# Optimization experiments

Measured on AMD Instinct MI355X. Metric: run time of the kernel, lower is better.

## Reference

```python
import jax, jax.numpy as jnp
import numpy as np

N_EMBD = 64
N_HEAD = 8
HEAD_SIZE = N_EMBD // N_HEAD  # 8
BLOCK_SIZE = 64
B = 4096
SCALE = N_EMBD ** (-0.5)  # NOTE: source scales by C**-0.5 with C=n_embd, not head_size
EPS = 1e-5


def setup_inputs() -> dict:
    key = jax.random.key(0)
    ks = jax.random.split(key, 12)
    s = 0.02
    return {
        "x": jax.random.normal(ks[0], (B, BLOCK_SIZE, N_EMBD), jnp.float32),
        # per-head q/k/v projections packed as [C, H, hs] (no bias in source)
        "Wq": jax.random.normal(ks[1], (N_EMBD, N_HEAD, HEAD_SIZE), jnp.float32) * s,
        "Wk": jax.random.normal(ks[2], (N_EMBD, N_HEAD, HEAD_SIZE), jnp.float32) * s,
        "Wv": jax.random.normal(ks[3], (N_EMBD, N_HEAD, HEAD_SIZE), jnp.float32) * s,
        "Wo": jax.random.normal(ks[4], (N_EMBD, N_EMBD), jnp.float32) * s,
        "bo": jnp.zeros((N_EMBD,), jnp.float32),
        "W1": jax.random.normal(ks[5], (N_EMBD, 4 * N_EMBD), jnp.float32) * s,
        "b1": jnp.zeros((4 * N_EMBD,), jnp.float32),
        "W2": jax.random.normal(ks[6], (4 * N_EMBD, N_EMBD), jnp.float32) * s,
        "b2": jnp.zeros((N_EMBD,), jnp.float32),
        "g1": jnp.ones((N_EMBD,), jnp.float32),
        "be1": jnp.zeros((N_EMBD,), jnp.float32),
        "g2": jnp.ones((N_EMBD,), jnp.float32),
        "be2": jnp.zeros((N_EMBD,), jnp.float32),
    }


def _layernorm(x, g, b):
    mu = jnp.mean(x, axis=-1, keepdims=True)
    var = jnp.mean(jnp.square(x - mu), axis=-1, keepdims=True)
    return (x - mu) * jax.lax.rsqrt(var + EPS) * g + b


def reference(x, Wq, Wk, Wv, Wo, bo, W1, b1, W2, b2, g1, be1, g2, be2):
    Bb, T, C = x.shape
    # --- multi-head causal self-attention (dropout = identity in eval) ---
    h = _layernorm(x, g1, be1)
    q = jnp.einsum('btc,chd->bhtd', h, Wq)
    k = jnp.einsum('btc,chd->bhtd', h, Wk)
    v = jnp.einsum('btc,chd->bhtd', h, Wv)
    wei = jnp.einsum('bhtd,bhsd->bhts', q, k) * SCALE
    mask = jnp.tril(jnp.ones((T, T), dtype=bool))
    wei = jnp.where(mask, wei, -jnp.inf)
    wei = jax.nn.softmax(wei, axis=-1)
    attn = jnp.einsum('bhts,bhsd->bhtd', wei, v)
    attn = attn.transpose(0, 2, 1, 3).reshape(Bb, T, C)  # concat heads
    x = x + attn @ Wo + bo
    # --- feed-forward ---
    h2 = _layernorm(x, g2, be2)
    ff = jax.nn.relu(h2 @ W1 + b1) @ W2 + b2
    return x + ff
```

## Files before the change

kernel.cpp:

```cpp
#include <hip/hip_runtime.h>
#include <hip/hip_bf16.h>


typedef __attribute__((ext_vector_type(8))) short short8;
typedef __attribute__((ext_vector_type(4))) float f32x4;

#if __has_builtin(__builtin_amdgcn_exp2f)
#define EXP2F(x) __builtin_amdgcn_exp2f(x)
#else
#define EXP2F(x) __expf((x) * 0.69314718056f)
#endif
#if __has_builtin(__builtin_amdgcn_rcpf)
#define RCPF(x) __builtin_amdgcn_rcpf(x)
#else
#define RCPF(x) (1.0f / (x))
#endif

#define ST  72
#define STU 264
#define OH  0
#define OQ  4608
#define OKK 9216
#define OV  13824
#define OP  18576
#define OU  9216
#define NSH 26112

__device__ __forceinline__ short f2bf(float f) {
    unsigned int u = __float_as_uint(f);
    u += 0x7fffu + ((u >> 16) & 1u);
    return (short)(u >> 16);
}
__device__ __forceinline__ unsigned pk2(float a, float b) {
    float2 t; t.x = a; t.y = b;
    __hip_bfloat162 h = __float22bfloat162_rn(t);
    unsigned u; __builtin_memcpy(&u, &h, 4); return u;
}
__device__ __forceinline__ f32x4 mfma16(short8 a, short8 b, f32x4 c) {
    return __builtin_amdgcn_mfma_f32_16x16x32_bf16(a, b, c, 0, 0, 0);
}

__global__ __launch_bounds__(256) void prepack_kernel(
    const float* __restrict__ Wq, const float* __restrict__ Wk,
    const float* __restrict__ Wv, const float* __restrict__ Wo,
    const float* __restrict__ W1, const float* __restrict__ W2,
    short* __restrict__ ws)
{
    int gid = blockIdx.x * 256 + threadIdx.x;
    int lane = gid & 63;
    int fid  = gid >> 6;
    int quad = lane >> 4, nn = lane & 15;
    short8 o;
    if (fid < 24) {
        int tile = fid >> 1, ks = fid & 1;
        const float* Ws = (tile < 4) ? Wq : ((tile < 8) ? Wk : Wv);
        float scale = (tile < 4) ? 0.18033688011f : 1.0f;
        int col = (tile & 3) * 16 + nn;
#pragma unroll
        for (int j = 0; j < 8; ++j)
            o[j] = f2bf(Ws[(ks * 32 + quad * 8 + j) * 64 + col] * scale);
    } else if (fid < 32) {
        int idx = fid - 24, nt = idx >> 1, ks = idx & 1;
#pragma unroll
        for (int j = 0; j < 8; ++j)
            o[j] = f2bf(Wo[(ks * 32 + quad * 8 + j) * 64 + nt * 16 + nn]);
    } else if (fid < 64) {
        int idx = fid - 32, c = idx >> 3, tile = (idx >> 1) & 3, ks = idx & 1;
#pragma unroll
        for (int j = 0; j < 8; ++j)
            o[j] = f2bf(W1[(ks * 32 + quad * 8 + j) * 256 + c * 64 + tile * 16 + nn]);
    } else {
        int idx = fid - 64, c = idx >> 3, nt = (idx >> 1) & 3, ks = idx & 1;
#pragma unroll
        for (int j = 0; j < 8; ++j)
            o[j] = f2bf(W2[(c * 64 + ks * 32 + quad * 8 + j) * 64 + nt * 16 + nn]);
    }
    *(short8*)(ws + (size_t)gid * 8) = o;
}

__global__ __launch_bounds__(256, 3) void block_kernel(
    const float* __restrict__ x,
    const float* __restrict__ bo,
    const float* __restrict__ b1,
    const float* __restrict__ b2,
    const float* __restrict__ g1, const float* __restrict__ be1,
    const float* __restrict__ g2, const float* __restrict__ be2,
    const short8* __restrict__ WB,
    float* __restrict__ out)
{
    __shared__ short sm[NSH];
    const int tid  = threadIdx.x;
    const int wv   = tid >> 6;
    const int lane = tid & 63;
    const int quad = lane >> 4;
    const int nn   = lane & 15;
    const int t_my = wv * 16 + nn;
    const int b    = blockIdx.x;
    const float* xb = x + (size_t)b * 4096;
    const f32x4 zf = {0.f, 0.f, 0.f, 0.f};
    const short8 z8 = {0, 0, 0, 0, 0, 0, 0, 0};

    if (tid < 144) sm[OV + 64 * ST + tid] = (tid < ST) ? (short)0x3F80 : (short)0;
    float xr[16];
    float gv[4], bv[4];
#pragma unroll
    for (int nt = 0; nt < 4; ++nt) { gv[nt] = g1[nt * 16 + nn]; bv[nt] = be1[nt * 16 + nn]; }
#pragma unroll
    for (int nt = 0; nt < 4; ++nt)
#pragma unroll
        for (int r = 0; r < 4; ++r)
            xr[nt * 4 + r] = xb[(wv * 16 + quad * 4 + r) * 64 + nt * 16 + nn];
#pragma unroll
    for (int r = 0; r < 4; ++r) {
        float s1 = 0.f, s2 = 0.f;
#pragma unroll
        for (int nt = 0; nt < 4; ++nt) { float v = xr[nt * 4 + r]; s1 += v; s2 += v * v; }
        s1 += __shfl_xor(s1, 1); s1 += __shfl_xor(s1, 2); s1 += __shfl_xor(s1, 4); s1 += __shfl_xor(s1, 8);
        s2 += __shfl_xor(s2, 1); s2 += __shfl_xor(s2, 2); s2 += __shfl_xor(s2, 4); s2 += __shfl_xor(s2, 8);
        float mu = s1 * 0.015625f;
        float rstd = rsqrtf(s2 * 0.015625f - mu * mu + 1e-5f);
        int base = OH + (wv * 16 + quad * 4 + r) * ST + nn;
        float v0 = (xr[0 * 4 + r] - mu) * rstd * gv[0] + bv[0];
        float v1 = (xr[1 * 4 + r] - mu) * rstd * gv[1] + bv[1];
        float v2 = (xr[2 * 4 + r] - mu) * rstd * gv[2] + bv[2];
        float v3 = (xr[3 * 4 + r] - mu) * rstd * gv[3] + bv[3];
        unsigned p01 = pk2(v0, v1), p23 = pk2(v2, v3);
        sm[base]      = (short)(p01 & 0xffff);
        sm[base + 16] = (short)(p01 >> 16);
        sm[base + 32] = (short)(p23 & 0xffff);
        sm[base + 48] = (short)(p23 >> 16);
    }

    {
        short8 hf0 = *(const short8*)&sm[OH + t_my * ST + quad * 8];
        short8 hf1 = *(const short8*)&sm[OH + t_my * ST + 32 + quad * 8];
#pragma unroll
        for (int jt = 0; jt < 4; ++jt) {
            f32x4 a = mfma16(WB[(size_t)(jt * 2 + 0) * 64 + lane], hf0, zf);
            a = mfma16(WB[(size_t)(jt * 2 + 1) * 64 + lane], hf1, a);
            uint2 w; w.x = pk2(a[0], a[1]); w.y = pk2(a[2], a[3]);
            *(uint2*)&sm[OQ + t_my * ST + jt * 16 + quad * 4] = w;
        }
#pragma unroll
        for (int jt = 0; jt < 4; ++jt) {
            f32x4 a = mfma16(WB[(size_t)((4 + jt) * 2 + 0) * 64 + lane], hf0, zf);
            a = mfma16(WB[(size_t)((4 + jt) * 2 + 1) * 64 + lane], hf1, a);
            uint2 w; w.x = pk2(a[0], a[1]); w.y = pk2(a[2], a[3]);
            *(uint2*)&sm[OKK + t_my * ST + jt * 16 + quad * 4] = w;
        }
#pragma unroll
        for (int dt = 0; dt < 4; ++dt) {
            f32x4 a = mfma16(hf0, WB[(size_t)((8 + dt) * 2 + 0) * 64 + lane], zf);
            a = mfma16(hf1, WB[(size_t)((8 + dt) * 2 + 1) * 64 + lane], a);
            uint2 w; w.x = pk2(a[0], a[1]); w.y = pk2(a[2], a[3]);
            *(uint2*)&sm[OV + (dt * 16 + nn) * ST + wv * 16 + quad * 4] = w;
        }
    }
    __syncthreads();

    const bool keep0 = (quad * 4 + 0) <= nn, keep1 = (quad * 4 + 1) <= nn;
    const bool keep2 = (quad * 4 + 2) <= nn, keep3 = (quad * 4 + 3) <= nn;
    const int arow_base = (nn < 8) ? nn : ((nn == 8) ? 64 : 65);
    const int arow_step = (nn < 8) ? 8 : 0;
    const int nks = (wv < 2) ? 1 : 2;
    const int zhi = nks * 2;
#pragma unroll 1
    for (int h = 0; h < 8; ++h) {
        short8 bq = z8;
        if (quad == 0) bq = *(const short8*)&sm[OQ + t_my * ST + h * 8];
        for (int mt = 0; mt <= wv; ++mt) {
            short8 ak = z8;
            if (quad == 0) ak = *(const short8*)&sm[OKK + (mt * 16 + nn) * ST + h * 8];
            f32x4 s = mfma16(ak, bq, zf);
            float e0 = EXP2F(s[0]), e1 = EXP2F(s[1]), e2 = EXP2F(s[2]), e3 = EXP2F(s[3]);
            if (mt == wv) {
                e0 = keep0 ? e0 : 0.f; e1 = keep1 ? e1 : 0.f;
                e2 = keep2 ? e2 : 0.f; e3 = keep3 ? e3 : 0.f;
            }
            uint2 w; w.x = pk2(e0, e1); w.y = pk2(e2, e3);
            *(uint2*)&sm[OP + t_my * ST + mt * 16 + quad * 4] = w;
        }
        for (int mt = wv + 1; mt < zhi; ++mt) {
            uint2 w; w.x = 0u; w.y = 0u;
            *(uint2*)&sm[OP + t_my * ST + mt * 16 + quad * 4] = w;
        }
        const int arow = arow_base + h * arow_step;
        f32x4 pv = zf;
        for (int ks = 0; ks < nks; ++ks) {
            short8 av = *(const short8*)&sm[OV + arow * ST + ks * 32 + quad * 8];
            short8 bp = *(const short8*)&sm[OP + t_my * ST + ks * 32 + quad * 8];
            pv = mfma16(av, bp, pv);
        }
        float denom = __shfl(pv[0], 32 + nn);
        float rd = RCPF(denom);
        if (quad < 2) {
            uint2 w; w.x = pk2(pv[0] * rd, pv[1] * rd); w.y = pk2(pv[2] * rd, pv[3] * rd);
            *(uint2*)&sm[OH + t_my * ST + h * 8 + quad * 4] = w;
        }
    }

    {
        short8 aa0 = *(const short8*)&sm[OH + t_my * ST + quad * 8];
        short8 aa1 = *(const short8*)&sm[OH + t_my * ST + 32 + quad * 8];
#pragma unroll
        for (int nt = 0; nt < 4; ++nt) {
            f32x4 oa = mfma16(aa0, WB[(size_t)(24 + nt * 2 + 0) * 64 + lane], zf);
            oa = mfma16(aa1, WB[(size_t)(24 + nt * 2 + 1) * 64 + lane], oa);
            float bov = bo[nt * 16 + nn];
#pragma unroll
            for (int r = 0; r < 4; ++r) xr[nt * 4 + r] += oa[r] + bov;
        }
    }
#pragma unroll
    for (int nt = 0; nt < 4; ++nt) { gv[nt] = g2[nt * 16 + nn]; bv[nt] = be2[nt * 16 + nn]; }
#pragma unroll
    for (int r = 0; r < 4; ++r) {
        float s1 = 0.f, s2 = 0.f;
#pragma unroll
        for (int nt = 0; nt < 4; ++nt) { float v = xr[nt * 4 + r]; s1 += v; s2 += v * v; }
        s1 += __shfl_xor(s1, 1); s1 += __shfl_xor(s1, 2); s1 += __shfl_xor(s1, 4); s1 += __shfl_xor(s1, 8);
        s2 += __shfl_xor(s2, 1); s2 += __shfl_xor(s2, 2); s2 += __shfl_xor(s2, 4); s2 += __shfl_xor(s2, 8);
        float mu = s1 * 0.015625f;
        float rstd = rsqrtf(s2 * 0.015625f - mu * mu + 1e-5f);
        int base = OQ + (wv * 16 + quad * 4 + r) * ST + nn;
        float v0 = (xr[0 * 4 + r] - mu) * rstd * gv[0] + bv[0];
        float v1 = (xr[1 * 4 + r] - mu) * rstd * gv[1] + bv[1];
        float v2 = (xr[2 * 4 + r] - mu) * rstd * gv[2] + bv[2];
        float v3 = (xr[3 * 4 + r] - mu) * rstd * gv[3] + bv[3];
        unsigned p01 = pk2(v0, v1), p23 = pk2(v2, v3);
        sm[base]      = (short)(p01 & 0xffff);
        sm[base + 16] = (short)(p01 >> 16);
        sm[base + 32] = (short)(p23 & 0xffff);
        sm[base + 48] = (short)(p23 >> 16);
    }

    short8 h2f0 = *(const short8*)&sm[OQ + t_my * ST + quad * 8];
    short8 h2f1 = *(const short8*)&sm[OQ + t_my * ST + 32 + quad * 8];
    __syncthreads();
#pragma unroll
    for (int c = 0; c < 4; ++c)
#pragma unroll
        for (int tile = 0; tile < 4; ++tile) {
            int fid = 32 + c * 8 + tile * 2;
            f32x4 u = mfma16(WB[(size_t)fid * 64 + lane], h2f0, zf);
            u = mfma16(WB[(size_t)(fid + 1) * 64 + lane], h2f1, u);
            const float4 bb = *(const float4*)&b1[c * 64 + tile * 16 + quad * 4];
            float u0 = fmaxf(u[0] + bb.x, 0.f), u1 = fmaxf(u[1] + bb.y, 0.f);
            float u2 = fmaxf(u[2] + bb.z, 0.f), u3 = fmaxf(u[3] + bb.w, 0.f);
            uint2 w; w.x = pk2(u0, u1); w.y = pk2(u2, u3);
            *(uint2*)&sm[OU + t_my * STU + c * 64 + tile * 16 + quad * 4] = w;
        }
    short8 uf[8];
#pragma unroll
    for (int ks = 0; ks < 8; ++ks)
        uf[ks] = *(const short8*)&sm[OU + t_my * STU + ks * 32 + quad * 8];
    f32x4 fa[4];
#pragma unroll
    for (int nt = 0; nt < 4; ++nt) fa[nt] = zf;
#pragma unroll
    for (int nt = 0; nt < 4; ++nt)
#pragma unroll
        for (int ks = 0; ks < 8; ++ks)
            fa[nt] = mfma16(uf[ks], WB[(size_t)(64 + (ks >> 1) * 8 + nt * 2 + (ks & 1)) * 64 + lane], fa[nt]);

    float* ob = out + (size_t)b * 4096;
#pragma unroll
    for (int nt = 0; nt < 4; ++nt) {
        float b2v = b2[nt * 16 + nn];
#pragma unroll
        for (int r = 0; r < 4; ++r)
            ob[(wv * 16 + quad * 4 + r) * 64 + nt * 16 + nn] = xr[nt * 4 + r] + fa[nt][r] + b2v;
    }
}

extern "C" void kernel_launch(void* const* d_in, const int* in_sizes, int n_in,
                              void* d_out, int out_size, void* d_ws, size_t ws_size,
                              hipStream_t stream) {
    const float* x   = (const float*)d_in[0];
    const float* Wq  = (const float*)d_in[1];
    const float* Wk  = (const float*)d_in[2];
    const float* Wv  = (const float*)d_in[3];
    const float* Wo  = (const float*)d_in[4];
    const float* bo  = (const float*)d_in[5];
    const float* W1  = (const float*)d_in[6];
    const float* b1  = (const float*)d_in[7];
    const float* W2  = (const float*)d_in[8];
    const float* b2  = (const float*)d_in[9];
    const float* g1  = (const float*)d_in[10];
    const float* be1 = (const float*)d_in[11];
    const float* g2  = (const float*)d_in[12];
    const float* be2 = (const float*)d_in[13];
    short* ws = (short*)d_ws;
    prepack_kernel<<<dim3(24), dim3(256), 0, stream>>>(Wq, Wk, Wv, Wo, W1, W2, ws);
    const int nb = in_sizes[0] / 4096;
    block_kernel<<<dim3(nb), dim3(256), 0, stream>>>(
        x, bo, b1, b2, g1, be1, g2, be2, (const short8*)ws, (float*)d_out);
}
```

Baseline: 206.4 us.

## Shrink shared memory footprint to raise occupancy to four blocks per CU

Q is kept in registers and broadcast through lane shuffles instead of being staged in shared memory. The FFN hidden activations are processed in two halves of 128 columns, so the U buffer shrinks and the second matmul is interleaved with the first. Shared memory drops from about 52KB to about 37KB, and launch bounds are raised to four blocks per CU to hide latency. The trade-offs are extra shuffles per head and tighter register pressure, and the weight prepack is relaunched with 64-thread blocks.

```diff
diff --git a/kernel.cpp b/kernel.cpp
--- a/kernel.cpp
+++ b/kernel.cpp
@@ -17,14 +17,13 @@
 #endif
 
 #define ST  72
-#define STU 264
+#define STU 136
 #define OH  0
-#define OQ  4608
-#define OKK 9216
-#define OV  13824
-#define OP  18576
-#define OU  9216
-#define NSH 26112
+#define OKK 4608
+#define OV  9216
+#define OP  13896
+#define OU  4608
+#define NSH 18504
 
 __device__ __forceinline__ short f2bf(float f) {
     unsigned int u = __float_as_uint(f);
@@ -40,13 +39,13 @@
     return __builtin_amdgcn_mfma_f32_16x16x32_bf16(a, b, c, 0, 0, 0);
 }
 
-__global__ __launch_bounds__(256) void prepack_kernel(
+__global__ __launch_bounds__(64) void prepack_kernel(
     const float* __restrict__ Wq, const float* __restrict__ Wk,
     const float* __restrict__ Wv, const float* __restrict__ Wo,
     const float* __restrict__ W1, const float* __restrict__ W2,
     short* __restrict__ ws)
 {
-    int gid = blockIdx.x * 256 + threadIdx.x;
+    int gid = blockIdx.x * 64 + threadIdx.x;
     int lane = gid & 63;
     int fid  = gid >> 6;
     int quad = lane >> 4, nn = lane & 15;
@@ -78,7 +77,7 @@
     *(short8*)(ws + (size_t)gid * 8) = o;
 }
 
-__global__ __launch_bounds__(256, 3) void block_kernel(
+__global__ __launch_bounds__(256, 4) void block_kernel(
     const float* __restrict__ x,
     const float* __restrict__ bo,
     const float* __restrict__ b1,
@@ -100,7 +99,7 @@
     const f32x4 zf = {0.f, 0.f, 0.f, 0.f};
     const short8 z8 = {0, 0, 0, 0, 0, 0, 0, 0};
 
-    if (tid < 144) sm[OV + 64 * ST + tid] = (tid < ST) ? (short)0x3F80 : (short)0;
+    if (tid < ST) sm[OV + 64 * ST + tid] = (short)0x3F80;
     float xr[16];
     float gv[4], bv[4];
 #pragma unroll
@@ -120,17 +119,12 @@
         float mu = s1 * 0.015625f;
         float rstd = rsqrtf(s2 * 0.015625f - mu * mu + 1e-5f);
         int base = OH + (wv * 16 + quad * 4 + r) * ST + nn;
-        float v0 = (xr[0 * 4 + r] - mu) * rstd * gv[0] + bv[0];
-        float v1 = (xr[1 * 4 + r] - mu) * rstd * gv[1] + bv[1];
-        float v2 = (xr[2 * 4 + r] - mu) * rstd * gv[2] + bv[2];
-        float v3 = (xr[3 * 4 + r] - mu) * rstd * gv[3] + bv[3];
-        unsigned p01 = pk2(v0, v1), p23 = pk2(v2, v3);
-        sm[base]      = (short)(p01 & 0xffff);
-        sm[base + 16] = (short)(p01 >> 16);
-        sm[base + 32] = (short)(p23 & 0xffff);
-        sm[base + 48] = (short)(p23 >> 16);
-    }
-
+#pragma unroll
+        for (int nt = 0; nt < 4; ++nt)
+            sm[base + nt * 16] = f2bf((xr[nt * 4 + r] - mu) * rstd * gv[nt] + bv[nt]);
+    }
+
+    unsigned qp[8];
     {
         short8 hf0 = *(const short8*)&sm[OH + t_my * ST + quad * 8];
         short8 hf1 = *(const short8*)&sm[OH + t_my * ST + 32 + quad * 8];
@@ -138,8 +132,8 @@
         for (int jt = 0; jt < 4; ++jt) {
             f32x4 a = mfma16(WB[(size_t)(jt * 2 + 0) * 64 + lane], hf0, zf);
             a = mfma16(WB[(size_t)(jt * 2 + 1) * 64 + lane], hf1, a);
-            uint2 w; w.x = pk2(a[0], a[1]); w.y = pk2(a[2], a[3]);
-            *(uint2*)&sm[OQ + t_my * ST + jt * 16 + quad * 4] = w;
+            qp[jt * 2 + 0] = pk2(a[0], a[1]);
+            qp[jt * 2 + 1] = pk2(a[2], a[3]);
         }
 #pragma unroll
         for (int jt = 0; jt < 4; ++jt) {
@@ -160,14 +154,23 @@
 
     const bool keep0 = (quad * 4 + 0) <= nn, keep1 = (quad * 4 + 1) <= nn;
     const bool keep2 = (quad * 4 + 2) <= nn, keep3 = (quad * 4 + 3) <= nn;
-    const int arow_base = (nn < 8) ? nn : ((nn == 8) ? 64 : 65);
+    const int arow_base = (nn < 8) ? nn : 64;
     const int arow_step = (nn < 8) ? 8 : 0;
     const int nks = (wv < 2) ? 1 : 2;
     const int zhi = nks * 2;
 #pragma unroll 1
     for (int h = 0; h < 8; ++h) {
-        short8 bq = z8;
-        if (quad == 0) bq = *(const short8*)&sm[OQ + t_my * ST + h * 8];
+        short8 bq;
+        {
+            int qsA = ((h & 1) * 2) * 16 + nn, qsB = qsA + 16;
+            int qi = (h >> 1) * 2;
+            union { unsigned u[4]; short8 s; } bb;
+            bb.u[0] = __shfl(qp[qi + 0], qsA);
+            bb.u[1] = __shfl(qp[qi + 1], qsA);
+            bb.u[2] = __shfl(qp[qi + 0], qsB);
+            bb.u[3] = __shfl(qp[qi + 1], qsB);
+            bq = bb.s;
+        }
         for (int mt = 0; mt <= wv; ++mt) {
             short8 ak = z8;
             if (quad == 0) ak = *(const short8*)&sm[OKK + (mt * 16 + nn) * ST + h * 8];
@@ -222,46 +225,42 @@
         s2 += __shfl_xor(s2, 1); s2 += __shfl_xor(s2, 2); s2 += __shfl_xor(s2, 4); s2 += __shfl_xor(s2, 8);
         float mu = s1 * 0.015625f;
         float rstd = rsqrtf(s2 * 0.015625f - mu * mu + 1e-5f);
-        int base = OQ + (wv * 16 + quad * 4 + r) * ST + nn;
-        float v0 = (xr[0 * 4 + r] - mu) * rstd * gv[0] + bv[0];
-        float v1 = (xr[1 * 4 + r] - mu) * rstd * gv[1] + bv[1];
-        float v2 = (xr[2 * 4 + r] - mu) * rstd * gv[2] + bv[2];
-        float v3 = (xr[3 * 4 + r] - mu) * rstd * gv[3] + bv[3];
-        unsigned p01 = pk2(v0, v1), p23 = pk2(v2, v3);
-        sm[base]      = (short)(p01 & 0xffff);
-        sm[base + 16] = (short)(p01 >> 16);
-        sm[base + 32] = (short)(p23 & 0xffff);
-        sm[base + 48] = (short)(p23 >> 16);
-    }
-
-    short8 h2f0 = *(const short8*)&sm[OQ + t_my * ST + quad * 8];
-    short8 h2f1 = *(const short8*)&sm[OQ + t_my * ST + 32 + quad * 8];
+        int base = OP + (wv * 16 + quad * 4 + r) * ST + nn;
+#pragma unroll
+        for (int nt = 0; nt < 4; ++nt)
+            sm[base + nt * 16] = f2bf((xr[nt * 4 + r] - mu) * rstd * gv[nt] + bv[nt]);
+    }
+    short8 h2f0 = *(const short8*)&sm[OP + t_my * ST + quad * 8];
+    short8 h2f1 = *(const short8*)&sm[OP + t_my * ST + 32 + quad * 8];
     __syncthreads();
-#pragma unroll
-    for (int c = 0; c < 4; ++c)
-#pragma unroll
-        for (int tile = 0; tile < 4; ++tile) {
-            int fid = 32 + c * 8 + tile * 2;
+
+    f32x4 fa[4];
+#pragma unroll
+    for (int nt = 0; nt < 4; ++nt) fa[nt] = zf;
+#pragma unroll
+    for (int c = 0; c < 2; ++c) {
+#pragma unroll
+        for (int tile = 0; tile < 8; ++tile) {
+            int gc = c * 8 + tile;
+            int fid = 32 + (gc >> 2) * 8 + (gc & 3) * 2;
             f32x4 u = mfma16(WB[(size_t)fid * 64 + lane], h2f0, zf);
             u = mfma16(WB[(size_t)(fid + 1) * 64 + lane], h2f1, u);
-            const float4 bb = *(const float4*)&b1[c * 64 + tile * 16 + quad * 4];
+            const float4 bb = *(const float4*)&b1[gc * 16 + quad * 4];
             float u0 = fmaxf(u[0] + bb.x, 0.f), u1 = fmaxf(u[1] + bb.y, 0.f);
             float u2 = fmaxf(u[2] + bb.z, 0.f), u3 = fmaxf(u[3] + bb.w, 0.f);
             uint2 w; w.x = pk2(u0, u1); w.y = pk2(u2, u3);
-            *(uint2*)&sm[OU + t_my * STU + c * 64 + tile * 16 + quad * 4] = w;
-        }
-    short8 uf[8];
-#pragma unroll
-    for (int ks = 0; ks < 8; ++ks)
-        uf[ks] = *(const short8*)&sm[OU + t_my * STU + ks * 32 + quad * 8];
-    f32x4 fa[4];
-#pragma unroll
-    for (int nt = 0; nt < 4; ++nt) fa[nt] = zf;
-#pragma unroll
-    for (int nt = 0; nt < 4; ++nt)
-#pragma unroll
-        for (int ks = 0; ks < 8; ++ks)
-            fa[nt] = mfma16(uf[ks], WB[(size_t)(64 + (ks >> 1) * 8 + nt * 2 + (ks & 1)) * 64 + lane], fa[nt]);
+            *(uint2*)&sm[OU + t_my * STU + tile * 16 + quad * 4] = w;
+        }
+#pragma unroll
+        for (int ks = 0; ks < 4; ++ks) {
+            short8 au = *(const short8*)&sm[OU + t_my * STU + ks * 32 + quad * 8];
+            int gk = c * 4 + ks;
+            int fidb = 64 + (gk >> 1) * 8 + (gk & 1);
+#pragma unroll
+            for (int nt = 0; nt < 4; ++nt)
+                fa[nt] = mfma16(au, WB[(size_t)(fidb + nt * 2) * 64 + lane], fa[nt]);
+        }
+    }
 
     float* ob = out + (size_t)b * 4096;
 #pragma unroll
@@ -291,7 +290,7 @@
     const float* g2  = (const float*)d_in[12];
     const float* be2 = (const float*)d_in[13];
     short* ws = (short*)d_ws;
-    prepack_kernel<<<dim3(24), dim3(256), 0, stream>>>(Wq, Wk, Wv, Wo, W1, W2, ws);
+    prepack_kernel<<<dim3(96), dim3(64), 0, stream>>>(Wq, Wk, Wv, Wo, W1, W2, ws);
     const int nb = in_sizes[0] / 4096;
     block_kernel<<<dim3(nb), dim3(256), 0, stream>>>(
         x, bo, b1, b2, g1, be1, g2, be2, (const short8*)ws, (float*)d_out);
```

New measurement: 202.2 us. -2.0%, faster.
